# Kernel tuning notes

Hardware: AMD Instinct MI355X
Metric: run time of the kernel (lower is better)

The kernel has to match this reference:

```python
import jax, jax.numpy as jnp
import numpy as np

# --- static architecture constants (match init_kwargs) ---
B, IH, IL, LH, E, FFH, NL = 256, 200, 6, 100, 256, 512, 2
G = IH + LH + 1  # 301 graph nodes
CLIP = 10.0


def setup_inputs() -> dict:
    key = jax.random.key(0)
    ks = jax.random.split(key, 24)

    # observation: 8 feature slots + trailing validity flag (all valid here)
    feats = jax.random.normal(ks[0], (B, G, 8), dtype=jnp.float32)
    valid = jnp.ones((B, G, 1), dtype=jnp.float32)
    observation = jnp.concatenate([feats, valid], axis=-1)  # [B, G, 9]

    def w(k, shape):
        fan_in = shape[-2] if len(shape) >= 2 else shape[0]
        return jax.random.normal(k, shape, dtype=jnp.float32) / np.sqrt(fan_in)

    return {
        "observation": observation,
        # per-node-type embedding MLPs (Linear -> LeakyReLU -> Linear)
        "wi1": w(ks[1], (IL, 32)), "bi1": jnp.zeros((32,), jnp.float32),
        "wi2": w(ks[2], (32, E)),  "bi2": jnp.zeros((E,), jnp.float32),
        "wl1": w(ks[3], (8, 32)),  "bl1": jnp.zeros((32,), jnp.float32),
        "wl2": w(ks[4], (32, E)),  "bl2": jnp.zeros((E,), jnp.float32),
        "wn1": w(ks[5], (6, 32)),  "bn1": jnp.zeros((32,), jnp.float32),
        "wn2": w(ks[6], (32, E)),  "bn2": jnp.zeros((E,), jnp.float32),
        # graph attention encoder, NL layers, weights stacked on axis 0
        "enc_wq": w(ks[7], (NL, E, E)),
        "enc_wk": w(ks[8], (NL, E, E)),
        "enc_wv": w(ks[9], (NL, E, E)),
        "enc_wo": w(ks[10], (NL, E, E)),
        "enc_wf1": w(ks[11], (NL, E, FFH)), "enc_bf1": jnp.zeros((NL, FFH), jnp.float32),
        "enc_wf2": w(ks[12], (NL, FFH, E)), "enc_bf2": jnp.zeros((NL, E), jnp.float32),
        # decoder projections (bias-free Linears)
        "w_pn": w(ks[13], (E, 3 * E)),  # project_node_embeddings
        "w_fc": w(ks[14], (E, E)),      # project_fixed_context
    }


def _ln(x):
    # normalization after skip connection (no affine)
    m = x.mean(-1, keepdims=True)
    v = x.var(-1, keepdims=True)
    return (x - m) * jax.lax.rsqrt(v + 1e-5)


def _mlp(x, w1, b1, w2, b2):
    return jax.nn.leaky_relu(x @ w1 + b1, 0.01) @ w2 + b2


def reference(observation, wi1, bi1, wi2, bi2, wl1, bl1, wl2, bl2,
              wn1, bn1, wn2, bn2, enc_wq, enc_wk, enc_wv, enc_wo,
              enc_wf1, enc_bf1, enc_wf2, enc_bf2, w_pn, w_fc):
    # --- observation_decode_leaf_node ---
    internal = observation[:, :IH, :IL]            # [B, IH, 6]
    leaf = observation[:, IH:IH + LH, :8]          # [B, LH, 8]
    nxt = observation[:, IH + LH:, :6]             # [B, 1, 6]
    leaf_valid = observation[:, IH:IH + LH, 8]     # [B, LH]
    full_mask = observation[:, :, 8]               # [B, G], 1 = valid
    leaf_mask = 1.0 - leaf_valid                   # 1 = invalid leaf
    valid_len = full_mask.sum(1)                   # [B]
    invalid = 1.0 - full_mask                      # full_mask_inv

    # --- initial per-node embeddings (normFactor = 1.0) ---
    h = jnp.concatenate([
        _mlp(internal, wi1, bi1, wi2, bi2),
        _mlp(leaf, wl1, bl1, wl2, bl2),
        _mlp(nxt, wn1, bn1, wn2, bn2),
    ], axis=1)                                     # [B, G, E]

    # --- graph self-attention encoder (n_heads=1, masked keys) ---
    attn_bias = invalid[:, None, :] * (-1e9)       # [B, 1, G]
    scale = 1.0 / np.sqrt(E)
    for l in range(NL):
        q = h @ enc_wq[l]
        k = h @ enc_wk[l]
        v = h @ enc_wv[l]
        scores = jnp.einsum('bqe,bke->bqk', q, k) * scale + attn_bias
        a = jax.nn.softmax(scores, axis=-1)        # [B, G, G]
        h = _ln(h + jnp.einsum('bqk,bke->bqe', a, v) @ enc_wo[l])
        h = _ln(h + jax.nn.relu(h @ enc_wf1[l] + enc_bf1[l]) @ enc_wf2[l] + enc_bf2[l])

    # --- _precompute: masked mean-pooled context + node projections ---
    trans = h * full_mask[:, :, None]              # zero invalid nodes
    graph_embed = trans.sum(1) / valid_len[:, None]
    fixed_context = graph_embed @ w_fc             # [B, E] query
    proj = trans @ w_pn                            # [B, G, 3E]
    glimpse_k = proj[..., :E]                      # logit_k/glimpse_v unused downstream

    # --- _one_to_many_logits (single head): q . k / sqrt(E), tanh clip ---
    compat = jnp.einsum('be,bge->bg', fixed_context, glimpse_k) * scale
    logits = jnp.tanh(compat) * CLIP
    logits = logits[:, IH:IH + LH]                 # leaf slice [B, LH]
    # mask_logits=False -> no -inf fill here

    # --- _get_log_p + _inner masking/renormalization ---
    p = jax.nn.softmax(logits, axis=-1)
    masked = p * (1.0 - leaf_mask) + 1e-20
    probs = masked / masked.sum(1, keepdims=True)  # [B, LH]
    return probs
```

## Files before the change

kernel.cpp:

```cpp
#include <hip/hip_runtime.h>
#include <math.h>

static constexpr int BB   = 256;
static constexpr int IHN  = 200;
static constexpr int ILN  = 6;
static constexpr int LHN  = 100;
static constexpr int EE   = 256;
static constexpr int FFH  = 512;
static constexpr int NL   = 2;
static constexpr int GG   = 301;
static constexpr int GP   = 320;
static constexpr int MT   = BB * GP;

typedef unsigned short u16;
typedef short bf16x8 __attribute__((ext_vector_type(8)));
typedef float f32x4 __attribute__((ext_vector_type(4)));

#define MFMA(a, b, c) __builtin_amdgcn_mfma_f32_16x16x32_bf16((a), (b), (c), 0, 0, 0)

__device__ __forceinline__ u16 f2bf(float f) {
    union { float f; unsigned u; } v; v.f = f;
    unsigned r = v.u + 0x7FFFu + ((v.u >> 16) & 1u);
    return (u16)(r >> 16);
}

__device__ __forceinline__ float waveReduceSum(float v) {
    for (int o = 32; o > 0; o >>= 1) v += __shfl_down(v, o, 64);
    return v;
}
__device__ __forceinline__ float waveReduceMax(float v) {
    for (int o = 32; o > 0; o >>= 1) v = fmaxf(v, __shfl_down(v, o, 64));
    return v;
}
__device__ __forceinline__ float blockReduceSum(float v, float* red) {
    int lane = threadIdx.x & 63;
    int w    = threadIdx.x >> 6;
    int nw   = (blockDim.x + 63) >> 6;
    v = waveReduceSum(v);
    if (lane == 0) red[w] = v;
    __syncthreads();
    if (threadIdx.x < 64) {
        float x = (lane < nw) ? red[lane] : 0.0f;
        x = waveReduceSum(x);
        if (lane == 0) red[0] = x;
    }
    __syncthreads();
    float r = red[0];
    __syncthreads();
    return r;
}
__device__ __forceinline__ float blockReduceMax(float v, float* red) {
    int lane = threadIdx.x & 63;
    int w    = threadIdx.x >> 6;
    int nw   = (blockDim.x + 63) >> 6;
    v = waveReduceMax(v);
    if (lane == 0) red[w] = v;
    __syncthreads();
    if (threadIdx.x < 64) {
        float x = (lane < nw) ? red[lane] : -INFINITY;
        x = waveReduceMax(x);
        if (lane == 0) red[0] = x;
    }
    __syncthreads();
    float r = red[0];
    __syncthreads();
    return r;
}

__device__ __forceinline__ void stage_swz(const u16* src, int strideShorts, int k0,
                                          u16* ldsTile, int nChunks, int wave,
                                          int nWaves, int lane)
{
    for (int c = wave; c < nChunks; c += nWaves) {
        int o = c * 1024 + lane * 16;
        int row = o >> 7;
        int cb = (o & 127) ^ ((row & 7) << 4);
        const u16* g = src + (size_t)row * strideShorts + k0 + (cb >> 1);
        __builtin_amdgcn_global_load_lds(
            (const __attribute__((address_space(1))) unsigned int*)g,
            (__attribute__((address_space(3))) unsigned int*)((char*)ldsTile + c * 1024),
            16, 0, 0);
    }
}

__device__ __forceinline__ bf16x8 lds_frag(const u16* tile, int row, int kk, int q)
{
    int cb = (kk * 64 + q * 16) ^ ((row & 7) << 4);
    return *(const bf16x8*)((const char*)tile + row * 128 + cb);
}

__global__ __launch_bounds__(256) void prep_kernel(
    const float* __restrict__ wq, const float* __restrict__ wk,
    const float* __restrict__ wv, const float* __restrict__ wo,
    const float* __restrict__ wf1, const float* __restrict__ wf2,
    u16* __restrict__ wT)
{
    int l = blockIdx.y / 6, m = blockIdx.y % 6;
    int idx = blockIdx.x * 256 + threadIdx.x;
    u16* dst = wT + (size_t)l * 524288;
    if (m < 4) {
        if (idx >= EE * EE) return;
        const float* src = (m == 0 ? wq : m == 1 ? wk : m == 2 ? wv : wo) + (size_t)l * EE * EE;
        int r = idx >> 8, c = idx & 255;
        dst[m * 65536 + idx] = f2bf(src[(size_t)c * EE + r]);
    } else if (m == 4) {
        if (idx >= FFH * EE) return;
        const float* src = wf1 + (size_t)l * EE * FFH;
        int r = idx >> 8, c = idx & 255;
        dst[262144 + idx] = f2bf(src[(size_t)c * FFH + r]);
    } else {
        if (idx >= EE * FFH) return;
        const float* src = wf2 + (size_t)l * FFH * EE;
        int r = idx >> 9, c = idx & 511;
        dst[393216 + idx] = f2bf(src[(size_t)c * EE + r]);
    }
}

template<int IND, int SEG, int G0>
__global__ __launch_bounds__(256) void embed_seg(
    const float* __restrict__ obs,
    const float* __restrict__ w1, const float* __restrict__ b1,
    const float* __restrict__ w2, const float* __restrict__ b2,
    float* __restrict__ h, u16* __restrict__ hb)
{
    __shared__ float xs[32][9];
    __shared__ float hid[32][33];
    int t = threadIdx.x;
    int fi0 = blockIdx.x * 32;

    for (int p = t; p < 32 * 9; p += 256) {
        int tok = p / 9, f = p % 9;
        int fi = fi0 + tok;
        int b = fi / SEG, g = G0 + fi % SEG;
        xs[tok][f] = obs[((size_t)b * GG + g) * 9 + f];
    }
    __syncthreads();

    #pragma unroll
    for (int p = 0; p < 4; p++) {
        int idx = p * 256 + t;
        int tok = idx >> 5, hcol = idx & 31;
        float a = b1[hcol];
        #pragma unroll
        for (int i = 0; i < IND; i++) a += xs[tok][i] * w1[i * 32 + hcol];
        hid[tok][hcol] = (a > 0.0f) ? a : 0.01f * a;
    }
    __syncthreads();

    float w2c[32];
    #pragma unroll
    for (int j = 0; j < 32; j++) w2c[j] = w2[j * EE + t];
    float bb = b2[t];
    for (int tok = 0; tok < 32; tok++) {
        int fi = fi0 + tok;
        int b = fi / SEG, g = G0 + fi % SEG;
        float a = bb;
        #pragma unroll
        for (int j = 0; j < 32; j++) a += hid[tok][j] * w2c[j];
        size_t o = ((size_t)b * GP + g) * EE + t;
        h[o] = a; hb[o] = f2bf(a);
    }
}

__global__ __launch_bounds__(256) void pad_kernel(float* __restrict__ h, u16* __restrict__ hb)
{
    int b = blockIdx.x, t = threadIdx.x;
    for (int g = GG; g < GP; g++) {
        size_t o = ((size_t)b * GP + g) * EE + t;
        h[o] = 0.0f; hb[o] = 0;
    }
}

__global__ __launch_bounds__(256) void qkv_gemm(
    const u16* __restrict__ hb, const u16* __restrict__ wqkvT,
    u16* __restrict__ qb, u16* __restrict__ kb, u16* __restrict__ vt)
{
    __shared__ __align__(16) u16 sA[2][128 * 64];
    __shared__ __align__(16) u16 sB[2][128 * 64];
    int tid = threadIdx.x, lane = tid & 63, w = tid >> 6;
    int wm = w >> 1, wn = w & 1;
    int lr = lane & 15, q = lane >> 4;
    int brow = blockIdx.x * 128;
    int bcol = blockIdx.y * 128;

    f32x4 acc[4][4];
    #pragma unroll
    for (int i = 0; i < 4; i++)
        #pragma unroll
        for (int j = 0; j < 4; j++) acc[i][j] = {0.0f, 0.0f, 0.0f, 0.0f};

    stage_swz(hb + (size_t)brow * 256, 256, 0, sA[0], 16, w, 4, lane);
    stage_swz(wqkvT + (size_t)bcol * 256, 256, 0, sB[0], 16, w, 4, lane);

    for (int ks = 0; ks < 4; ks++) {
        int cur = ks & 1;
        if (ks < 3) {
            stage_swz(hb + (size_t)brow * 256, 256, (ks + 1) * 64, sA[cur ^ 1], 16, w, 4, lane);
            stage_swz(wqkvT + (size_t)bcol * 256, 256, (ks + 1) * 64, sB[cur ^ 1], 16, w, 4, lane);
            asm volatile("s_waitcnt vmcnt(8)" ::: "memory");
        } else {
            asm volatile("s_waitcnt vmcnt(0)" ::: "memory");
        }
        __builtin_amdgcn_s_barrier();
        #pragma unroll
        for (int kk = 0; kk < 2; kk++) {
            bf16x8 a[4], b[4];
            #pragma unroll
            for (int i = 0; i < 4; i++) {
                a[i] = lds_frag(sA[cur], wm * 64 + i * 16 + lr, kk, q);
                b[i] = lds_frag(sB[cur], wn * 64 + i * 16 + lr, kk, q);
            }
            #pragma unroll
            for (int mi = 0; mi < 4; mi++)
                #pragma unroll
                for (int ni = 0; ni < 4; ni++)
                    acc[mi][ni] = MFMA(a[mi], b[ni], acc[mi][ni]);
        }
        __builtin_amdgcn_sched_barrier(0);
        __builtin_amdgcn_s_barrier();
    }

    if (bcol < 512) {
        u16* dst = (bcol < 256) ? qb : kb;
        int cOff = bcol & 255;
        #pragma unroll
        for (int mi = 0; mi < 4; mi++)
            #pragma unroll
            for (int ni = 0; ni < 4; ni++) {
                int col = cOff + wn * 64 + ni * 16 + lr;
                #pragma unroll
                for (int j = 0; j < 4; j++) {
                    int rowG = brow + wm * 64 + mi * 16 + q * 4 + j;
                    dst[(size_t)rowG * 256 + col] = f2bf(acc[mi][ni][j]);
                }
            }
    } else {
        #pragma unroll
        for (int mi = 0; mi < 4; mi++) {
            int rowG0 = brow + wm * 64 + mi * 16 + q * 4;
            int b0 = rowG0 / GP;
            int g0 = rowG0 - b0 * GP;
            #pragma unroll
            for (int ni = 0; ni < 4; ni++) {
                int e = (bcol - 512) + wn * 64 + ni * 16 + lr;
                ushort4 u4;
                u4.x = f2bf(acc[mi][ni][0]);
                u4.y = f2bf(acc[mi][ni][1]);
                u4.z = f2bf(acc[mi][ni][2]);
                u4.w = f2bf(acc[mi][ni][3]);
                *(ushort4*)(vt + ((size_t)(b0 * EE + e)) * GP + g0) = u4;
            }
        }
    }
}

__global__ __launch_bounds__(256) void ff1_gemm(
    const u16* __restrict__ hb, const u16* __restrict__ w1T,
    const float* __restrict__ bf1, u16* __restrict__ hidb)
{
    __shared__ __align__(16) u16 sA[2][128 * 64];
    __shared__ __align__(16) u16 sB[2][128 * 64];
    int tid = threadIdx.x, lane = tid & 63, w = tid >> 6;
    int wm = w >> 1, wn = w & 1;
    int lr = lane & 15, q = lane >> 4;
    int brow = blockIdx.x * 128;
    int bcol = blockIdx.y * 128;

    f32x4 acc[4][4];
    #pragma unroll
    for (int i = 0; i < 4; i++)
        #pragma unroll
        for (int j = 0; j < 4; j++) acc[i][j] = {0.0f, 0.0f, 0.0f, 0.0f};

    stage_swz(hb + (size_t)brow * 256, 256, 0, sA[0], 16, w, 4, lane);
    stage_swz(w1T + (size_t)bcol * 256, 256, 0, sB[0], 16, w, 4, lane);

    for (int ks = 0; ks < 4; ks++) {
        int cur = ks & 1;
        if (ks < 3) {
            stage_swz(hb + (size_t)brow * 256, 256, (ks + 1) * 64, sA[cur ^ 1], 16, w, 4, lane);
            stage_swz(w1T + (size_t)bcol * 256, 256, (ks + 1) * 64, sB[cur ^ 1], 16, w, 4, lane);
            asm volatile("s_waitcnt vmcnt(8)" ::: "memory");
        } else {
            asm volatile("s_waitcnt vmcnt(0)" ::: "memory");
        }
        __builtin_amdgcn_s_barrier();
        #pragma unroll
        for (int kk = 0; kk < 2; kk++) {
            bf16x8 a[4], b[4];
            #pragma unroll
            for (int i = 0; i < 4; i++) {
                a[i] = lds_frag(sA[cur], wm * 64 + i * 16 + lr, kk, q);
                b[i] = lds_frag(sB[cur], wn * 64 + i * 16 + lr, kk, q);
            }
            #pragma unroll
            for (int mi = 0; mi < 4; mi++)
                #pragma unroll
                for (int ni = 0; ni < 4; ni++)
                    acc[mi][ni] = MFMA(a[mi], b[ni], acc[mi][ni]);
        }
        __builtin_amdgcn_sched_barrier(0);
        __builtin_amdgcn_s_barrier();
    }

    #pragma unroll
    for (int ni = 0; ni < 4; ni++) {
        int col = bcol + wn * 64 + ni * 16 + lr;
        float bias = bf1[col];
        #pragma unroll
        for (int mi = 0; mi < 4; mi++)
            #pragma unroll
            for (int j = 0; j < 4; j++) {
                int rowG = brow + wm * 64 + mi * 16 + q * 4 + j;
                float v = acc[mi][ni][j] + bias;
                hidb[(size_t)rowG * 512 + col] = f2bf(fmaxf(v, 0.0f));
            }
    }
}

template<int KSTEPS, int STR, bool HASB>
__global__ __launch_bounds__(512) void gemmln_kernel(
    const u16* __restrict__ A, const u16* __restrict__ Bw,
    const float* __restrict__ bias, float* __restrict__ h, u16* __restrict__ hb)
{
    __shared__ __align__(16) u16 sA[2][64 * 64];
    __shared__ __align__(16) u16 sB[2][256 * 64];
    int tid = threadIdx.x, lane = tid & 63, w = tid >> 6;
    int wm = w >> 2, wn = w & 3;
    int lr = lane & 15, q = lane >> 4;
    int brow = blockIdx.x * 64;

    f32x4 acc[2][4];
    #pragma unroll
    for (int i = 0; i < 2; i++)
        #pragma unroll
        for (int j = 0; j < 4; j++) acc[i][j] = {0.0f, 0.0f, 0.0f, 0.0f};

    stage_swz(A + (size_t)brow * STR, STR, 0, sA[0], 8, w, 8, lane);
    stage_swz(Bw, STR, 0, sB[0], 32, w, 8, lane);

    for (int ks = 0; ks < KSTEPS; ks++) {
        int cur = ks & 1;
        if (ks + 1 < KSTEPS) {
            stage_swz(A + (size_t)brow * STR, STR, (ks + 1) * 64, sA[cur ^ 1], 8, w, 8, lane);
            stage_swz(Bw, STR, (ks + 1) * 64, sB[cur ^ 1], 32, w, 8, lane);
            asm volatile("s_waitcnt vmcnt(5)" ::: "memory");
        } else {
            asm volatile("s_waitcnt vmcnt(0)" ::: "memory");
        }
        __builtin_amdgcn_s_barrier();
        #pragma unroll
        for (int kk = 0; kk < 2; kk++) {
            bf16x8 a[2], b[4];
            #pragma unroll
            for (int i = 0; i < 2; i++)
                a[i] = lds_frag(sA[cur], wm * 32 + i * 16 + lr, kk, q);
            #pragma unroll
            for (int n = 0; n < 4; n++)
                b[n] = lds_frag(sB[cur], wn * 64 + n * 16 + lr, kk, q);
            #pragma unroll
            for (int mi = 0; mi < 2; mi++)
                #pragma unroll
                for (int ni = 0; ni < 4; ni++)
                    acc[mi][ni] = MFMA(a[mi], b[ni], acc[mi][ni]);
        }
        __builtin_amdgcn_sched_barrier(0);
        __builtin_amdgcn_s_barrier();
    }

    __syncthreads();
    float* sPart = (float*)sA;

    #pragma unroll
    for (int ni = 0; ni < 4; ni++) {
        int col = wn * 64 + ni * 16 + lr;
        float bv = HASB ? bias[col] : 0.0f;
        #pragma unroll
        for (int mi = 0; mi < 2; mi++)
            #pragma unroll
            for (int j = 0; j < 4; j++) {
                int rowG = brow + wm * 32 + mi * 16 + q * 4 + j;
                acc[mi][ni][j] += bv + h[(size_t)rowG * 256 + col];
            }
    }
    #pragma unroll
    for (int mi = 0; mi < 2; mi++)
        #pragma unroll
        for (int j = 0; j < 4; j++) {
            float s1 = 0.0f, s2 = 0.0f;
            #pragma unroll
            for (int ni = 0; ni < 4; ni++) {
                float v = acc[mi][ni][j];
                s1 += v; s2 += v * v;
            }
            s1 += __shfl_xor(s1, 1); s2 += __shfl_xor(s2, 1);
            s1 += __shfl_xor(s1, 2); s2 += __shfl_xor(s2, 2);
            s1 += __shfl_xor(s1, 4); s2 += __shfl_xor(s2, 4);
            s1 += __shfl_xor(s1, 8); s2 += __shfl_xor(s2, 8);
            if (lr == 0) {
                int lrow = wm * 32 + mi * 16 + q * 4 + j;
                sPart[(wn * 64 + lrow) * 2 + 0] = s1;
                sPart[(wn * 64 + lrow) * 2 + 1] = s2;
            }
        }
    __syncthreads();

    #pragma unroll
    for (int mi = 0; mi < 2; mi++)
        #pragma unroll
        for (int j = 0; j < 4; j++) {
            int lrow = wm * 32 + mi * 16 + q * 4 + j;
            float s1 = sPart[lrow * 2] + sPart[(64 + lrow) * 2] +
                       sPart[(128 + lrow) * 2] + sPart[(192 + lrow) * 2];
            float s2 = sPart[lrow * 2 + 1] + sPart[(64 + lrow) * 2 + 1] +
                       sPart[(128 + lrow) * 2 + 1] + sPart[(192 + lrow) * 2 + 1];
            float mean = s1 * (1.0f / 256.0f);
            float var  = s2 * (1.0f / 256.0f) - mean * mean;
            float rstd = rsqrtf(var + 1e-5f);
            int rowG = brow + lrow;
            #pragma unroll
            for (int ni = 0; ni < 4; ni++) {
                int col = wn * 64 + ni * 16 + lr;
                float v = (acc[mi][ni][j] - mean) * rstd;
                size_t o = (size_t)rowG * 256 + col;
                h[o] = v; hb[o] = f2bf(v);
            }
        }
}

__global__ __launch_bounds__(512) void attn_core(
    const u16* __restrict__ qb, const u16* __restrict__ kb,
    const u16* __restrict__ vt, const float* __restrict__ obs,
    u16* __restrict__ aob)
{
    __shared__ __align__(16) u16 sKV[2][16384];
    __shared__ __align__(16) u16 sPt[64 * 72];
    __shared__ float sBias[320];
    __shared__ float sPm[2][64], sPs[2][64];

    int id = blockIdx.x;
    int xcd = id & 7, jj = id >> 3;
    int tile = jj % 5, bgrp = jj / 5;
    int b = xcd + 8 * bgrp;
    int t0 = tile * 64;

    int tid = threadIdx.x, w = tid >> 6, lane = tid & 63;
    int wm = w >> 1, wn = w & 1;
    int lr = lane & 15, q = lane >> 4, lk = q * 8;

    if (tid < 320) {
        float msk = (tid < GG) ? obs[((size_t)b * GG + tid) * 9 + 8] : 0.0f;
        sBias[tid] = (1.0f - msk) * -1e9f;
    }

    const u16* qbase = qb + ((size_t)(b * GP + t0 + wm * 16 + lr)) * 256;
    bf16x8 af[8];
    #pragma unroll
    for (int k8 = 0; k8 < 8; k8++) af[k8] = *(const bf16x8*)(qbase + k8 * 32 + lk);

    const u16* vbase = vt + (size_t)b * EE * GP;

    #pragma unroll
    for (int r = 0; r < 4; r++)
        stage_swz(kb + ((size_t)b * GP) * 256, 256, r * 64, sKV[0] + r * 4096, 8, w, 8, lane);

    f32x4 sacc[10];
    #pragma unroll
    for (int s = 0; s < 10; s++) sacc[s] = {0.0f, 0.0f, 0.0f, 0.0f};

    #pragma unroll
    for (int t = 0; t < 5; t++) {
        if (t < 4) {
            #pragma unroll
            for (int r = 0; r < 4; r++)
                stage_swz(kb + ((size_t)(b * GP + (t + 1) * 64)) * 256, 256, r * 64,
                          sKV[(t + 1) & 1] + r * 4096, 8, w, 8, lane);
            asm volatile("s_waitcnt vmcnt(4)" ::: "memory");
        } else {
            asm volatile("s_waitcnt vmcnt(0)" ::: "memory");
        }
        __builtin_amdgcn_s_barrier();
        const u16* kbuf = sKV[t & 1];
        #pragma unroll
        for (int ks = 0; ks < 4; ks++)
            #pragma unroll
            for (int kk = 0; kk < 2; kk++) {
                bf16x8 a = af[ks * 2 + kk];
                #pragma unroll
                for (int l = 0; l < 2; l++) {
                    int jl = (wn * 2 + l) * 16 + lr;
                    bf16x8 bb = lds_frag(kbuf + ks * 4096, jl, kk, q);
                    sacc[t * 2 + l] = MFMA(a, bb, sacc[t * 2 + l]);
                }
            }
        __builtin_amdgcn_s_barrier();
    }

    #pragma unroll
    for (int s = 0; s < 10; s++) {
        int j = (s >> 1) * 64 + (wn * 2 + (s & 1)) * 16 + lr;
        float bia = sBias[j];
        #pragma unroll
        for (int r = 0; r < 4; r++) sacc[s][r] = sacc[s][r] * 0.0625f + bia;
    }
    #pragma unroll
    for (int r = 0; r < 4; r++) {
        float mx = -1e30f;
        #pragma unroll
        for (int s = 0; s < 10; s++) mx = fmaxf(mx, sacc[s][r]);
        mx = fmaxf(mx, __shfl_xor(mx, 1));
        mx = fmaxf(mx, __shfl_xor(mx, 2));
        mx = fmaxf(mx, __shfl_xor(mx, 4));
        mx = fmaxf(mx, __shfl_xor(mx, 8));
        if (lr == 0) sPm[wn][wm * 16 + q * 4 + r] = mx;
    }
    __syncthreads();

    stage_swz(vbase, GP, 0 * 64, sKV[0], 32, w, 8, lane);

    #pragma unroll
    for (int r = 0; r < 4; r++) {
        int row = wm * 16 + q * 4 + r;
        float rm = fmaxf(sPm[0][row], sPm[1][row]);
        float ss = 0.0f;
        #pragma unroll
        for (int s = 0; s < 10; s++) {
            float e = __expf(sacc[s][r] - rm);
            sacc[s][r] = e;
            ss += e;
        }
        ss += __shfl_xor(ss, 1);
        ss += __shfl_xor(ss, 2);
        ss += __shfl_xor(ss, 4);
        ss += __shfl_xor(ss, 8);
        if (lr == 0) sPs[wn][row] = ss;
    }
    asm volatile("s_waitcnt lgkmcnt(0)" ::: "memory");
    __builtin_amdgcn_s_barrier();
    __builtin_amdgcn_sched_barrier(0);

    float invr[4];
    #pragma unroll
    for (int r = 0; r < 4; r++) {
        int row = wm * 16 + q * 4 + r;
        invr[r] = 1.0f / (sPs[0][row] + sPs[1][row]);
    }
    unsigned pk[10][2];
    #pragma unroll
    for (int s = 0; s < 10; s++) {
        pk[s][0] = (unsigned)f2bf(sacc[s][0] * invr[0]) |
                   ((unsigned)f2bf(sacc[s][1] * invr[1]) << 16);
        pk[s][1] = (unsigned)f2bf(sacc[s][2] * invr[2]) |
                   ((unsigned)f2bf(sacc[s][3] * invr[3]) << 16);
    }

    f32x4 oacc[8];
    #pragma unroll
    for (int n = 0; n < 8; n++) oacc[n] = {0.0f, 0.0f, 0.0f, 0.0f};

    #pragma unroll
    for (int c = 0; c < 5; c++) {
        if (c < 4) {
            stage_swz(vbase, GP, (c + 1) * 64, sKV[(c + 1) & 1], 32, w, 8, lane);
            asm volatile("s_waitcnt vmcnt(4)" ::: "memory");
        } else {
            asm volatile("s_waitcnt vmcnt(0)" ::: "memory");
        }
        __builtin_amdgcn_s_barrier();
        #pragma unroll
        for (int sl = 0; sl < 2; sl++) {
            int jl = (wn * 2 + sl) * 16 + lr;
            #pragma unroll
            for (int r = 0; r < 4; r++) {
                int row = wm * 16 + q * 4 + r;
                unsigned v = pk[c * 2 + sl][r >> 1];
                sPt[row * 72 + jl] = (u16)((r & 1) ? (v >> 16) : (v & 0xffffu));
            }
        }
        asm volatile("s_waitcnt lgkmcnt(0)" ::: "memory");
        __builtin_amdgcn_s_barrier();
        __builtin_amdgcn_sched_barrier(0);
        #pragma unroll
        for (int kk = 0; kk < 2; kk++) {
            bf16x8 a = *(const bf16x8*)(sPt + (wm * 16 + lr) * 72 + kk * 32 + lk);
            #pragma unroll
            for (int n = 0; n < 8; n++) {
                bf16x8 vv = lds_frag(sKV[c & 1], wn * 128 + n * 16 + lr, kk, q);
                oacc[n] = MFMA(a, vv, oacc[n]);
            }
        }
        __builtin_amdgcn_s_barrier();
    }

    #pragma unroll
    for (int n = 0; n < 8; n++) {
        int col = wn * 128 + n * 16 + lr;
        #pragma unroll
        for (int r = 0; r < 4; r++) {
            int row = wm * 16 + q * 4 + r;
            aob[((size_t)(b * GP + t0 + row)) * 256 + col] = f2bf(oacc[n][r]);
        }
    }
}

__global__ __launch_bounds__(256) void final1_kernel(
    const float* __restrict__ h, const float* __restrict__ obs,
    const float* __restrict__ w_fc, const float* __restrict__ w_pn,
    float* __restrict__ u)
{
    int b = blockIdx.x;
    int t = threadIdx.x;
    __shared__ float ges[EE];
    __shared__ float fcs[EE];

    float acc = 0.0f, vlen = 0.0f;
    for (int g = 0; g < GG; g++) {
        float m = obs[((size_t)b * GG + g) * 9 + 8];
        vlen += m;
        acc += h[((size_t)b * GP + g) * EE + t] * m;
    }
    ges[t] = acc / vlen;
    __syncthreads();

    float fc = 0.0f;
    for (int kk = 0; kk < EE; kk++) fc += ges[kk] * w_fc[kk * EE + t];
    fcs[t] = fc;
    __syncthreads();

    const float4* wp = reinterpret_cast<const float4*>(w_pn + (size_t)t * 3 * EE);
    float ua = 0.0f;
    for (int kk = 0; kk < EE / 4; kk++) {
        float4 w = wp[kk];
        ua += w.x * fcs[kk * 4] + w.y * fcs[kk * 4 + 1] +
              w.z * fcs[kk * 4 + 2] + w.w * fcs[kk * 4 + 3];
    }
    u[(size_t)b * EE + t] = ua;
}

__global__ __launch_bounds__(128) void final2_kernel(
    const float* __restrict__ h, const float* __restrict__ obs,
    const float* __restrict__ u, float* __restrict__ out)
{
    int b = blockIdx.x;
    int t = threadIdx.x;
    __shared__ float us[EE];
    __shared__ float red[8];
    us[t]       = u[(size_t)b * EE + t];
    us[t + 128] = u[(size_t)b * EE + t + 128];
    __syncthreads();

    float logit = -INFINITY;
    float m = 0.0f;
    if (t < LHN) {
        int g = IHN + t;
        m = obs[((size_t)b * GG + g) * 9 + 8];
        const float4* hr = reinterpret_cast<const float4*>(h + ((size_t)b * GP + g) * EE);
        float c = 0.0f;
        for (int kk = 0; kk < EE / 4; kk++) {
            float4 hv = hr[kk];
            c += hv.x * us[kk * 4] + hv.y * us[kk * 4 + 1] +
                 hv.z * us[kk * 4 + 2] + hv.w * us[kk * 4 + 3];
        }
        c *= m;
        c *= 0.0625f;
        logit = tanhf(c) * 10.0f;
    }
    float bm = blockReduceMax(logit, red);
    float e  = (t < LHN) ? __expf(logit - bm) : 0.0f;
    float bs = blockReduceSum(e, red);
    float p  = e / bs;
    float masked = (t < LHN) ? (p * m + 1e-20f) : 0.0f;
    float bs2 = blockReduceSum(masked, red);
    if (t < LHN) out[(size_t)b * LHN + t] = masked / bs2;
}

extern "C" void kernel_launch(void* const* d_in, const int* in_sizes, int n_in,
                              void* d_out, int out_size, void* d_ws, size_t ws_size,
                              hipStream_t stream) {
    const float* obs   = (const float*)d_in[0];
    const float* wi1   = (const float*)d_in[1];
    const float* bi1   = (const float*)d_in[2];
    const float* wi2   = (const float*)d_in[3];
    const float* bi2   = (const float*)d_in[4];
    const float* wl1   = (const float*)d_in[5];
    const float* bl1   = (const float*)d_in[6];
    const float* wl2   = (const float*)d_in[7];
    const float* bl2   = (const float*)d_in[8];
    const float* wn1   = (const float*)d_in[9];
    const float* bn1   = (const float*)d_in[10];
    const float* wn2   = (const float*)d_in[11];
    const float* bn2   = (const float*)d_in[12];
    const float* e_wq  = (const float*)d_in[13];
    const float* e_wk  = (const float*)d_in[14];
    const float* e_wv  = (const float*)d_in[15];
    const float* e_wo  = (const float*)d_in[16];
    const float* e_wf1 = (const float*)d_in[17];
    const float* e_bf1 = (const float*)d_in[18];
    const float* e_wf2 = (const float*)d_in[19];
    const float* e_bf2 = (const float*)d_in[20];
    const float* w_pn  = (const float*)d_in[21];
    const float* w_fc  = (const float*)d_in[22];
    float* outp = (float*)d_out;

    char* wsc = (char*)d_ws;
    float* h    = (float*)wsc;
    u16*   hb   = (u16*)(wsc + 83886080);
    u16*   qaob = (u16*)(wsc + 125829120);
    u16*   kb   = (u16*)(wsc + 167772160);
    u16*   vt   = (u16*)(wsc + 209715200);
    u16*   wT   = (u16*)(wsc + 251658240);
    float* ubuf = (float*)(wsc + 253755392);
    u16*   hidb = kb;

    prep_kernel<<<dim3(512, 12), 256, 0, stream>>>(e_wq, e_wk, e_wv, e_wo, e_wf1, e_wf2, wT);
    pad_kernel<<<BB, 256, 0, stream>>>(h, hb);
    embed_seg<ILN, IHN, 0><<<IHN * BB / 32, 256, 0, stream>>>(obs, wi1, bi1, wi2, bi2, h, hb);
    embed_seg<8, LHN, IHN><<<LHN * BB / 32, 256, 0, stream>>>(obs, wl1, bl1, wl2, bl2, h, hb);
    embed_seg<6, 1, IHN + LHN><<<BB / 32, 256, 0, stream>>>(obs, wn1, bn1, wn2, bn2, h, hb);

    const size_t WL = 524288;
    for (int l = 0; l < NL; l++) {
        u16* wqkvT = wT + l * WL;
        u16* woT   = wqkvT + 196608;
        u16* w1T   = wqkvT + 262144;
        u16* w2T   = wqkvT + 393216;
        const float* bf1 = e_bf1 + (size_t)l * FFH;
        const float* bf2 = e_bf2 + (size_t)l * EE;

        qkv_gemm<<<dim3(MT / 128, 6), 256, 0, stream>>>(hb, wqkvT, qaob, kb, vt);
        attn_core<<<1280, 512, 0, stream>>>(qaob, kb, vt, obs, qaob);
        gemmln_kernel<4, 256, false><<<MT / 64, 512, 0, stream>>>(qaob, woT, nullptr, h, hb);
        ff1_gemm<<<dim3(MT / 128, 4), 256, 0, stream>>>(hb, w1T, bf1, hidb);
        gemmln_kernel<8, 512, true><<<MT / 64, 512, 0, stream>>>(hidb, w2T, bf2, h, hb);
    }
    final1_kernel<<<BB, 256, 0, stream>>>(h, obs, w_fc, w_pn, ubuf);
    final2_kernel<<<BB, 128, 0, stream>>>(h, obs, ubuf, outp);
}
```

Before: 700.3 us.

## Keep A rows in registers and stream weight tiles across full N in QKV/FF1 GEMMs

The QKV and FF1 GEMMs now launch one 512-thread block per 128-row tile instead of a 2D grid over column tiles. Each wave holds its 16 rows of A (full K=256) in registers and loops over all output column tiles, double-buffering 64-column weight slabs through LDS. This avoids re-reading the activation matrix once per column tile and drops the A staging through LDS. The trade-off is fewer blocks, higher register pressure, and lower MFMA reuse per B fragment, since each wave has only a 16-row tile.

```diff
diff --git a/kernel.cpp b/kernel.cpp
--- a/kernel.cpp
+++ b/kernel.cpp
@@ -171,150 +171,138 @@
     }
 }
 
-__global__ __launch_bounds__(256) void qkv_gemm(
+__global__ __launch_bounds__(512) void qkv_gemm(
     const u16* __restrict__ hb, const u16* __restrict__ wqkvT,
     u16* __restrict__ qb, u16* __restrict__ kb, u16* __restrict__ vt)
 {
-    __shared__ __align__(16) u16 sA[2][128 * 64];
-    __shared__ __align__(16) u16 sB[2][128 * 64];
+    __shared__ __align__(16) u16 sB[2][16384];
     int tid = threadIdx.x, lane = tid & 63, w = tid >> 6;
-    int wm = w >> 1, wn = w & 1;
-    int lr = lane & 15, q = lane >> 4;
+    int lr = lane & 15, q = lane >> 4, lk = q * 8;
     int brow = blockIdx.x * 128;
-    int bcol = blockIdx.y * 128;
-
-    f32x4 acc[4][4];
-    #pragma unroll
-    for (int i = 0; i < 4; i++)
-        #pragma unroll
-        for (int j = 0; j < 4; j++) acc[i][j] = {0.0f, 0.0f, 0.0f, 0.0f};
-
-    stage_swz(hb + (size_t)brow * 256, 256, 0, sA[0], 16, w, 4, lane);
-    stage_swz(wqkvT + (size_t)bcol * 256, 256, 0, sB[0], 16, w, 4, lane);
-
-    for (int ks = 0; ks < 4; ks++) {
-        int cur = ks & 1;
-        if (ks < 3) {
-            stage_swz(hb + (size_t)brow * 256, 256, (ks + 1) * 64, sA[cur ^ 1], 16, w, 4, lane);
-            stage_swz(wqkvT + (size_t)bcol * 256, 256, (ks + 1) * 64, sB[cur ^ 1], 16, w, 4, lane);
-            asm volatile("s_waitcnt vmcnt(8)" ::: "memory");
+
+    const u16* abase = hb + ((size_t)(brow + w * 16 + lr)) * 256;
+    bf16x8 af[8];
+    #pragma unroll
+    for (int k8 = 0; k8 < 8; k8++) af[k8] = *(const bf16x8*)(abase + k8 * 32 + lk);
+
+    int rowG0 = brow + w * 16 + q * 4;
+    int b0 = rowG0 / GP, g0 = rowG0 - b0 * GP;
+
+    #pragma unroll
+    for (int r = 0; r < 4; r++)
+        stage_swz(wqkvT, 256, r * 64, sB[0] + r * 4096, 8, w, 8, lane);
+
+    for (int nt = 0; nt < 12; nt++) {
+        int cur = nt & 1;
+        if (nt < 11) {
+            #pragma unroll
+            for (int r = 0; r < 4; r++)
+                stage_swz(wqkvT + (size_t)(nt + 1) * 64 * 256, 256, r * 64,
+                          sB[cur ^ 1] + r * 4096, 8, w, 8, lane);
+            asm volatile("s_waitcnt vmcnt(4)" ::: "memory");
         } else {
             asm volatile("s_waitcnt vmcnt(0)" ::: "memory");
         }
         __builtin_amdgcn_s_barrier();
-        #pragma unroll
-        for (int kk = 0; kk < 2; kk++) {
-            bf16x8 a[4], b[4];
-            #pragma unroll
-            for (int i = 0; i < 4; i++) {
-                a[i] = lds_frag(sA[cur], wm * 64 + i * 16 + lr, kk, q);
-                b[i] = lds_frag(sB[cur], wn * 64 + i * 16 + lr, kk, q);
-            }
-            #pragma unroll
-            for (int mi = 0; mi < 4; mi++)
+
+        f32x4 acc[4];
+        #pragma unroll
+        for (int n = 0; n < 4; n++) acc[n] = {0.0f, 0.0f, 0.0f, 0.0f};
+        #pragma unroll
+        for (int k8 = 0; k8 < 8; k8++) {
+            bf16x8 a = af[k8];
+            #pragma unroll
+            for (int n = 0; n < 4; n++) {
+                bf16x8 bb = lds_frag(sB[cur] + (k8 >> 1) * 4096, n * 16 + lr, k8 & 1, q);
+                acc[n] = MFMA(a, bb, acc[n]);
+            }
+        }
+
+        if (nt < 8) {
+            u16* dst = (nt < 4) ? qb : kb;
+            int cOff = (nt & 3) * 64;
+            #pragma unroll
+            for (int n = 0; n < 4; n++) {
+                int col = cOff + n * 16 + lr;
                 #pragma unroll
-                for (int ni = 0; ni < 4; ni++)
-                    acc[mi][ni] = MFMA(a[mi], b[ni], acc[mi][ni]);
+                for (int j = 0; j < 4; j++)
+                    dst[(size_t)(rowG0 + j) * 256 + col] = f2bf(acc[n][j]);
+            }
+        } else {
+            #pragma unroll
+            for (int n = 0; n < 4; n++) {
+                int e = (nt - 8) * 64 + n * 16 + lr;
+                ushort4 u4;
+                u4.x = f2bf(acc[n][0]);
+                u4.y = f2bf(acc[n][1]);
+                u4.z = f2bf(acc[n][2]);
+                u4.w = f2bf(acc[n][3]);
+                *(ushort4*)(vt + ((size_t)(b0 * EE + e)) * GP + g0) = u4;
+            }
         }
         __builtin_amdgcn_sched_barrier(0);
         __builtin_amdgcn_s_barrier();
     }
-
-    if (bcol < 512) {
-        u16* dst = (bcol < 256) ? qb : kb;
-        int cOff = bcol & 255;
-        #pragma unroll
-        for (int mi = 0; mi < 4; mi++)
-            #pragma unroll
-            for (int ni = 0; ni < 4; ni++) {
-                int col = cOff + wn * 64 + ni * 16 + lr;
-                #pragma unroll
-                for (int j = 0; j < 4; j++) {
-                    int rowG = brow + wm * 64 + mi * 16 + q * 4 + j;
-                    dst[(size_t)rowG * 256 + col] = f2bf(acc[mi][ni][j]);
-                }
-            }
-    } else {
-        #pragma unroll
-        for (int mi = 0; mi < 4; mi++) {
-            int rowG0 = brow + wm * 64 + mi * 16 + q * 4;
-            int b0 = rowG0 / GP;
-            int g0 = rowG0 - b0 * GP;
-            #pragma unroll
-            for (int ni = 0; ni < 4; ni++) {
-                int e = (bcol - 512) + wn * 64 + ni * 16 + lr;
-                ushort4 u4;
-                u4.x = f2bf(acc[mi][ni][0]);
-                u4.y = f2bf(acc[mi][ni][1]);
-                u4.z = f2bf(acc[mi][ni][2]);
-                u4.w = f2bf(acc[mi][ni][3]);
-                *(ushort4*)(vt + ((size_t)(b0 * EE + e)) * GP + g0) = u4;
-            }
-        }
-    }
-}
-
-__global__ __launch_bounds__(256) void ff1_gemm(
+}
+
+__global__ __launch_bounds__(512) void ff1_gemm(
     const u16* __restrict__ hb, const u16* __restrict__ w1T,
     const float* __restrict__ bf1, u16* __restrict__ hidb)
 {
-    __shared__ __align__(16) u16 sA[2][128 * 64];
-    __shared__ __align__(16) u16 sB[2][128 * 64];
+    __shared__ __align__(16) u16 sB[2][16384];
     int tid = threadIdx.x, lane = tid & 63, w = tid >> 6;
-    int wm = w >> 1, wn = w & 1;
-    int lr = lane & 15, q = lane >> 4;
+    int lr = lane & 15, q = lane >> 4, lk = q * 8;
     int brow = blockIdx.x * 128;
-    int bcol = blockIdx.y * 128;
-
-    f32x4 acc[4][4];
-    #pragma unroll
-    for (int i = 0; i < 4; i++)
-        #pragma unroll
-        for (int j = 0; j < 4; j++) acc[i][j] = {0.0f, 0.0f, 0.0f, 0.0f};
-
-    stage_swz(hb + (size_t)brow * 256, 256, 0, sA[0], 16, w, 4, lane);
-    stage_swz(w1T + (size_t)bcol * 256, 256, 0, sB[0], 16, w, 4, lane);
-
-    for (int ks = 0; ks < 4; ks++) {
-        int cur = ks & 1;
-        if (ks < 3) {
-            stage_swz(hb + (size_t)brow * 256, 256, (ks + 1) * 64, sA[cur ^ 1], 16, w, 4, lane);
-            stage_swz(w1T + (size_t)bcol * 256, 256, (ks + 1) * 64, sB[cur ^ 1], 16, w, 4, lane);
-            asm volatile("s_waitcnt vmcnt(8)" ::: "memory");
+
+    const u16* abase = hb + ((size_t)(brow + w * 16 + lr)) * 256;
+    bf16x8 af[8];
+    #pragma unroll
+    for (int k8 = 0; k8 < 8; k8++) af[k8] = *(const bf16x8*)(abase + k8 * 32 + lk);
+
+    int rowG0 = brow + w * 16 + q * 4;
+
+    #pragma unroll
+    for (int r = 0; r < 4; r++)
+        stage_swz(w1T, 256, r * 64, sB[0] + r * 4096, 8, w, 8, lane);
+
+    for (int nt = 0; nt < 8; nt++) {
+        int cur = nt & 1;
+        if (nt < 7) {
+            #pragma unroll
+            for (int r = 0; r < 4; r++)
+                stage_swz(w1T + (size_t)(nt + 1) * 64 * 256, 256, r * 64,
+                          sB[cur ^ 1] + r * 4096, 8, w, 8, lane);
+            asm volatile("s_waitcnt vmcnt(4)" ::: "memory");
         } else {
             asm volatile("s_waitcnt vmcnt(0)" ::: "memory");
         }
         __builtin_amdgcn_s_barrier();
-        #pragma unroll
-        for (int kk = 0; kk < 2; kk++) {
-            bf16x8 a[4], b[4];
-            #pragma unroll
-            for (int i = 0; i < 4; i++) {
-                a[i] = lds_frag(sA[cur], wm * 64 + i * 16 + lr, kk, q);
-                b[i] = lds_frag(sB[cur], wn * 64 + i * 16 + lr, kk, q);
-            }
-            #pragma unroll
-            for (int mi = 0; mi < 4; mi++)
-                #pragma unroll
-                for (int ni = 0; ni < 4; ni++)
-                    acc[mi][ni] = MFMA(a[mi], b[ni], acc[mi][ni]);
+
+        f32x4 acc[4];
+        #pragma unroll
+        for (int n = 0; n < 4; n++) acc[n] = {0.0f, 0.0f, 0.0f, 0.0f};
+        #pragma unroll
+        for (int k8 = 0; k8 < 8; k8++) {
+            bf16x8 a = af[k8];
+            #pragma unroll
+            for (int n = 0; n < 4; n++) {
+                bf16x8 bb = lds_frag(sB[cur] + (k8 >> 1) * 4096, n * 16 + lr, k8 & 1, q);
+                acc[n] = MFMA(a, bb, acc[n]);
+            }
+        }
+
+        #pragma unroll
+        for (int n = 0; n < 4; n++) {
+            int col = nt * 64 + n * 16 + lr;
+            float bias = bf1[col];
+            #pragma unroll
+            for (int j = 0; j < 4; j++) {
+                float v = acc[n][j] + bias;
+                hidb[(size_t)(rowG0 + j) * 512 + col] = f2bf(fmaxf(v, 0.0f));
+            }
         }
         __builtin_amdgcn_sched_barrier(0);
         __builtin_amdgcn_s_barrier();
-    }
-
-    #pragma unroll
-    for (int ni = 0; ni < 4; ni++) {
-        int col = bcol + wn * 64 + ni * 16 + lr;
-        float bias = bf1[col];
-        #pragma unroll
-        for (int mi = 0; mi < 4; mi++)
-            #pragma unroll
-            for (int j = 0; j < 4; j++) {
-                int rowG = brow + wm * 64 + mi * 16 + q * 4 + j;
-                float v = acc[mi][ni][j] + bias;
-                hidb[(size_t)rowG * 512 + col] = f2bf(fmaxf(v, 0.0f));
-            }
     }
 }
 
@@ -727,10 +715,10 @@
         const float* bf1 = e_bf1 + (size_t)l * FFH;
         const float* bf2 = e_bf2 + (size_t)l * EE;
 
-        qkv_gemm<<<dim3(MT / 128, 6), 256, 0, stream>>>(hb, wqkvT, qaob, kb, vt);
+        qkv_gemm<<<MT / 128, 512, 0, stream>>>(hb, wqkvT, qaob, kb, vt);
         attn_core<<<1280, 512, 0, stream>>>(qaob, kb, vt, obs, qaob);
         gemmln_kernel<4, 256, false><<<MT / 64, 512, 0, stream>>>(qaob, woT, nullptr, h, hb);
-        ff1_gemm<<<dim3(MT / 128, 4), 256, 0, stream>>>(hb, w1T, bf1, hidb);
+        ff1_gemm<<<MT / 128, 512, 0, stream>>>(hb, w1T, bf1, hidb);
         gemmln_kernel<8, 512, true><<<MT / 64, 512, 0, stream>>>(hidb, w2T, bf2, h, hb);
     }
     final1_kernel<<<BB, 256, 0, stream>>>(h, obs, w_fc, w_pn, ubuf);
```

Result: faster. 626.0 us, median of 2 (-10.6%).
